# Kernel tuning notes

Hardware: AMD Instinct MI355X
Metric: run time of the kernel (lower is better)

The kernel has to match this reference:

```python
import jax, jax.numpy as jnp
import numpy as np

N = 100000
E = 1600000
F_IN = 128
HID = 64
N_CLS = 16


def gcn_conv(x, row, col, W, b, n_nodes):
    # x: [N, Fin]; row/col: [E+N] (self-loops already appended)
    h = x @ W  # [N, Fout]
    ones = jnp.ones(row.shape[0], dtype=x.dtype)
    deg = jax.ops.segment_sum(ones, col, num_segments=n_nodes)  # in-degree incl. self-loop
    dinv = jnp.where(deg > 0, jax.lax.rsqrt(deg), 0.0)
    norm = dinv[row] * dinv[col]  # [E+N]
    msg = h[row] * norm[:, None]  # gather + scale
    out = jax.ops.segment_sum(msg, col, num_segments=n_nodes)  # scatter-add
    return out + b


def setup_inputs() -> dict:
    key = jax.random.key(0)
    k1, k2, k3, k4, k5, k6 = jax.random.split(key, 6)
    x = jax.random.normal(k1, (N, F_IN), dtype=jnp.float32)
    edge_index = jax.random.randint(k2, (2, E), 0, N, dtype=jnp.int64)
    # Glorot-ish init for weights
    W1 = jax.random.normal(k3, (F_IN, HID), dtype=jnp.float32) / np.sqrt(F_IN)
    b1 = jnp.zeros((HID,), dtype=jnp.float32)
    W2 = jax.random.normal(k4, (HID, N_CLS), dtype=jnp.float32) / np.sqrt(HID)
    b2 = jnp.zeros((N_CLS,), dtype=jnp.float32)
    return {"x": x, "edge_index": edge_index, "W1": W1, "b1": b1, "W2": W2, "b2": b2}


def reference(x, edge_index, W1, b1, W2, b2):
    # Add self-loops (GCNConv default add_self_loops=True)
    loop = jnp.arange(N, dtype=edge_index.dtype)
    row = jnp.concatenate([edge_index[0], loop])
    col = jnp.concatenate([edge_index[1], loop])
    h = gcn_conv(x, row, col, W1, b1, N)
    h = jax.nn.relu(h)
    h = gcn_conv(h, row, col, W2, b2, N)
    return jax.nn.log_softmax(h, axis=1)
```

## Files before the change

kernel.cpp:

```cpp
#include <hip/hip_runtime.h>
#include <hip/hip_fp16.h>

#define F_IN 128
#define HID  64
#define NCLS 16
#define NPB  128
#define CHUNK 4096
#define BINTHREADS 1024
#define GPAD 136

typedef _Float16 half_t;
typedef __attribute__((ext_vector_type(4))) _Float16 half4;
typedef __attribute__((ext_vector_type(8))) _Float16 half8;
typedef __attribute__((ext_vector_type(4))) float float4v;


__global__ __launch_bounds__(BINTHREADS) void bucket_hist(const int* __restrict__ col,
                                                          int* __restrict__ tot, int E, int NB) {
    __shared__ int hist[1024];
    for (int i = threadIdx.x; i < NB; i += BINTHREADS) hist[i] = 0;
    __syncthreads();
    int e0 = blockIdx.x * CHUNK;
    #pragma unroll
    for (int j = 0; j < CHUNK / BINTHREADS; ++j) {
        int e = e0 + j * BINTHREADS + threadIdx.x;
        if (e < E) atomicAdd(&hist[col[e] >> 7], 1);
    }
    __syncthreads();
    for (int i = threadIdx.x; i < NB; i += BINTHREADS)
        if (hist[i]) atomicAdd(&tot[i], hist[i]);
}


__global__ __launch_bounds__(256) void bucket_scan(const int* __restrict__ tot,
                                                   int* __restrict__ base, int* __restrict__ cursor,
                                                   int* __restrict__ row_start, int NB, int N, int E) {
    __shared__ int s[256];
    int t = threadIdx.x, i0 = t * 4;
    int v0 = (i0 + 0 < NB) ? tot[i0 + 0] : 0;
    int v1 = (i0 + 1 < NB) ? tot[i0 + 1] : 0;
    int v2 = (i0 + 2 < NB) ? tot[i0 + 2] : 0;
    int v3 = (i0 + 3 < NB) ? tot[i0 + 3] : 0;
    int tsum = v0 + v1 + v2 + v3;
    s[t] = tsum;
    __syncthreads();
    for (int off = 1; off < 256; off <<= 1) {
        int x = (t >= off) ? s[t - off] : 0;
        __syncthreads();
        s[t] += x;
        __syncthreads();
    }
    int run = s[t] - tsum;
    if (i0 + 0 < NB) { base[i0 + 0] = run; cursor[i0 + 0] = run; } run += v0;
    if (i0 + 1 < NB) { base[i0 + 1] = run; cursor[i0 + 1] = run; } run += v1;
    if (i0 + 2 < NB) { base[i0 + 2] = run; cursor[i0 + 2] = run; } run += v2;
    if (i0 + 3 < NB) { base[i0 + 3] = run; cursor[i0 + 3] = run; }
    if (t == 0) { base[NB] = E; row_start[N] = E; }
}


__global__ __launch_bounds__(BINTHREADS) void phaseA(const int* __restrict__ row, const int* __restrict__ col,
                                                     int* __restrict__ cursor, int* __restrict__ ebuf,
                                                     int E, int NB) {
    __shared__ int hist[1024], base[1024], off[1024];
    for (int i = threadIdx.x; i < NB; i += BINTHREADS) hist[i] = 0;
    __syncthreads();
    int e0 = blockIdx.x * CHUNK;
    #pragma unroll
    for (int j = 0; j < CHUNK / BINTHREADS; ++j) {
        int e = e0 + j * BINTHREADS + threadIdx.x;
        if (e < E) atomicAdd(&hist[col[e] >> 7], 1);
    }
    __syncthreads();
    for (int i = threadIdx.x; i < NB; i += BINTHREADS) {
        int h = hist[i];
        base[i] = h ? atomicAdd(&cursor[i], h) : 0;
        off[i] = 0;
    }
    __syncthreads();
    #pragma unroll
    for (int j = 0; j < CHUNK / BINTHREADS; ++j) {
        int e = e0 + j * BINTHREADS + threadIdx.x;
        if (e < E) {
            int c = col[e], b = c >> 7;
            int p = base[b] + atomicAdd(&off[b], 1);
            ebuf[p] = (row[e] << 7) | (c & (NPB - 1));
        }
    }
}


__global__ __launch_bounds__(256) void phaseB(const int* __restrict__ ebuf, const int* __restrict__ bbase,
                                              int* __restrict__ row_start, int* __restrict__ csr_row,
                                              float* __restrict__ dinv, int N) {
    __shared__ int hist[NPB], sc[NPB], cur[NPB];
    int t = threadIdx.x;
    int node0 = blockIdx.x << 7;
    int e0 = bbase[blockIdx.x], e1 = bbase[blockIdx.x + 1];
    if (t < NPB) hist[t] = 0;
    __syncthreads();
    for (int e = e0 + t; e < e1; e += 256) atomicAdd(&hist[ebuf[e] & (NPB - 1)], 1);
    __syncthreads();
    if (t < NPB) sc[t] = hist[t];
    __syncthreads();
    for (int off = 1; off < NPB; off <<= 1) {
        int x = (t < NPB && t >= off) ? sc[t - off] : 0;
        __syncthreads();
        if (t < NPB) sc[t] += x;
        __syncthreads();
    }
    if (t < NPB) {
        int start = e0 + sc[t] - hist[t];
        cur[t] = start;
        int n = node0 + t;
        if (n < N) {
            row_start[n] = start;
            dinv[n] = rsqrtf((float)hist[t] + 1.0f);
        }
    }
    __syncthreads();
    for (int e = e0 + t; e < e1; e += 256) {
        int p = ebuf[e];
        int pos = atomicAdd(&cur[p & (NPB - 1)], 1);
        csr_row[pos] = p >> 7;
    }
}


__global__ void prep_w1(const float* __restrict__ W1, half_t* __restrict__ W1t) {
    int i = blockIdx.x * 256 + threadIdx.x;
    if (i < F_IN * HID) {
        int k = i >> 6, n = i & 63;
        W1t[n * F_IN + k] = (half_t)W1[i];
    }
}


__global__ __launch_bounds__(256) void gemm1(
    const float* __restrict__ x, const half_t* __restrict__ W1t,
    const float* __restrict__ dinv, __half* __restrict__ hs1, int N)
{
    __shared__ __align__(16) half_t As[16 * GPAD + 8];
    int node0 = blockIdx.x * 16;
    size_t total = (size_t)N * F_IN;
    for (int idx = threadIdx.x; idx < 16 * F_IN / 4; idx += 256) {
        int nl = idx >> 5;
        int k4 = idx & 31;
        size_t g = (size_t)(node0 + nl) * F_IN + k4 * 4;
        float4 v = make_float4(0.f, 0.f, 0.f, 0.f);
        if (g < total) v = *(const float4*)&x[g];
        half_t* dst = &As[nl * GPAD + k4 * 4];
        dst[0] = (half_t)v.x; dst[1] = (half_t)v.y;
        dst[2] = (half_t)v.z; dst[3] = (half_t)v.w;
    }
    __syncthreads();
    int wv = threadIdx.x >> 6, lane = threadIdx.x & 63;
    int l15 = lane & 15, quad = lane >> 4;
    int fcol = wv * 16 + l15;
    float4v acc = {0.f, 0.f, 0.f, 0.f};
    #pragma unroll
    for (int kb = 0; kb < 4; ++kb) {
        half8 a = *(const half8*)&As[l15 * GPAD + kb * 32 + quad * 8];
        half8 b = *(const half8*)&W1t[(size_t)fcol * F_IN + kb * 32 + quad * 8];
        acc = __builtin_amdgcn_mfma_f32_16x16x32_f16(a, b, acc, 0, 0, 0);
    }
    #pragma unroll
    for (int r = 0; r < 4; ++r) {
        int node = node0 + quad * 4 + r;
        if (node < N) hs1[(size_t)node * HID + fcol] = __float2half(acc[r] * dinv[node]);
    }
}


__global__ __launch_bounds__(256) void agg_l1(
    const __half* __restrict__ hs1, const int* __restrict__ rs,
    const int* __restrict__ csr, const float* __restrict__ dinv,
    const float* __restrict__ b1, const float* __restrict__ W2,
    __half* __restrict__ h2s, int N)
{
    __shared__ float W2l[HID * NCLS];
    __shared__ float o1[16][65];
    for (int i = threadIdx.x; i < HID * NCLS; i += 256) W2l[i] = W2[i];
    __syncthreads();
    int w = threadIdx.x >> 6, lane = threadIdx.x & 63;
    int g = lane >> 4, gl = lane & 15;
    int rowi = w * 4 + g;
    int c = blockIdx.x * 16 + rowi;
    bool active = (c < N);
    int cc = active ? c : 0;
    float dc = dinv[cc];
    int e0 = rs[cc], e1 = rs[cc + 1];
    int e1m1 = e1 - 1;
    const half4* H = (const half4*)hs1;
    half4 sv = H[(size_t)cc * 16 + gl];
    float4 sum = make_float4((float)sv[0], (float)sv[1], (float)sv[2], (float)sv[3]);
    for (int i = e0; i < e1; i += 8) {
        int id[8];
        #pragma unroll
        for (int s = 0; s < 8; ++s) id[s] = csr[min(i + s, e1m1)];
        half4 a[8];
        #pragma unroll
        for (int s = 0; s < 8; ++s) a[s] = H[(size_t)id[s] * 16 + gl];
        #pragma unroll
        for (int s = 0; s < 8; ++s) {
            float fm = (i + s < e1) ? 1.f : 0.f;
            sum.x = fmaf(fm, (float)a[s][0], sum.x);
            sum.y = fmaf(fm, (float)a[s][1], sum.y);
            sum.z = fmaf(fm, (float)a[s][2], sum.z);
            sum.w = fmaf(fm, (float)a[s][3], sum.w);
        }
    }
    float4 bb = *(const float4*)&b1[gl * 4];
    o1[rowi][gl * 4 + 0] = fmaxf(fmaf(dc, sum.x, bb.x), 0.f);
    o1[rowi][gl * 4 + 1] = fmaxf(fmaf(dc, sum.y, bb.y), 0.f);
    o1[rowi][gl * 4 + 2] = fmaxf(fmaf(dc, sum.z, bb.z), 0.f);
    o1[rowi][gl * 4 + 3] = fmaxf(fmaf(dc, sum.w, bb.w), 0.f);
    float s16 = 0.f;
    const float* orow = o1[rowi];
    #pragma unroll 8
    for (int k = 0; k < HID; ++k) s16 = fmaf(orow[k], W2l[k * NCLS + gl], s16);
    if (active) h2s[(size_t)c * NCLS + gl] = __float2half(dc * s16);
}


__global__ __launch_bounds__(256) void agg2_final(
    const __half* __restrict__ h2s, const int* __restrict__ rs,
    const int* __restrict__ csr, const float* __restrict__ dinv,
    const float* __restrict__ b2, float* __restrict__ out, int N)
{
    int lane = threadIdx.x & 63;
    int g = lane >> 3, gl = lane & 7;
    int c = blockIdx.x * 32 + (threadIdx.x >> 6) * 8 + g;
    bool active = (c < N);
    int cc = active ? c : 0;
    float dcv = dinv[cc];
    int e0 = rs[cc], e1 = rs[cc + 1];
    int e1m1 = e1 - 1;
    const __half2* H = (const __half2*)h2s;
    float2 sum = __half22float2(H[(size_t)cc * 8 + gl]);
    for (int i = e0; i < e1; i += 8) {
        int id[8];
        #pragma unroll
        for (int s = 0; s < 8; ++s) id[s] = csr[min(i + s, e1m1)];
        __half2 a[8];
        #pragma unroll
        for (int s = 0; s < 8; ++s) a[s] = H[(size_t)id[s] * 8 + gl];
        #pragma unroll
        for (int s = 0; s < 8; ++s) {
            float fm = (i + s < e1) ? 1.f : 0.f;
            float2 f2 = __half22float2(a[s]);
            sum.x = fmaf(fm, f2.x, sum.x);
            sum.y = fmaf(fm, f2.y, sum.y);
        }
    }
    float2 bb = ((const float2*)b2)[gl];
    float2 v;
    v.x = fmaf(dcv, sum.x, bb.x);
    v.y = fmaf(dcv, sum.y, bb.y);
    float mx = fmaxf(v.x, v.y);
    mx = fmaxf(mx, __shfl_xor(mx, 1, 64));
    mx = fmaxf(mx, __shfl_xor(mx, 2, 64));
    mx = fmaxf(mx, __shfl_xor(mx, 4, 64));
    float s = __expf(v.x - mx) + __expf(v.y - mx);
    s += __shfl_xor(s, 1, 64);
    s += __shfl_xor(s, 2, 64);
    s += __shfl_xor(s, 4, 64);
    float lse = mx + __logf(s);
    if (active) ((float2*)out)[(size_t)c * 8 + gl] = make_float2(v.x - lse, v.y - lse);
}


extern "C" void kernel_launch(void* const* d_in, const int* in_sizes, int n_in,
                              void* d_out, int out_size, void* d_ws, size_t ws_size,
                              hipStream_t stream) {
    const float* x  = (const float*)d_in[0];
    const int*   ei = (const int*)d_in[1];
    const float* W1 = (const float*)d_in[2];
    const float* b1 = (const float*)d_in[3];
    const float* W2 = (const float*)d_in[4];
    const float* b2 = (const float*)d_in[5];
    float* out = (float*)d_out;

    const int N = in_sizes[0] / F_IN;
    const int E = in_sizes[1] / 2;
    const int* row = ei;
    const int* col = ei + E;

    const int NB = (N + NPB - 1) / NPB;
    size_t Np  = ((size_t)N + 15) & ~(size_t)15;
    size_t Ep  = ((size_t)E + 15) & ~(size_t)15;
    size_t NBp = ((size_t)NB + 15) & ~(size_t)15;

    char* p = (char*)d_ws;
    float*  dinv      = (float*)p;   p += Np * 4;
    __half* hs1       = (__half*)p;  p += Np * HID * 2;
    __half* h2s       = (__half*)p;  p += Np * NCLS * 2;
    half_t* W1t       = (half_t*)p;  p += (size_t)F_IN * HID * 2;
    int*    row_start = (int*)p;     p += (Np + 16) * 4;
    int*    csr_row   = (int*)p;     p += Ep * 4;
    int*    ebuf      = (int*)p;     p += Ep * 4;
    int*    btot      = (int*)p;     p += NBp * 4;
    int*    bbase     = (int*)p;     p += (NBp + 16) * 4;
    int*    bcur      = (int*)p;     p += NBp * 4;

    int nblkE = (E + CHUNK - 1) / CHUNK;

    hipMemsetAsync(btot, 0, NBp * sizeof(int), stream);
    bucket_hist<<<nblkE, BINTHREADS, 0, stream>>>(col, btot, E, NB);
    bucket_scan<<<1, 256, 0, stream>>>(btot, bbase, bcur, row_start, NB, N, E);
    phaseA<<<nblkE, BINTHREADS, 0, stream>>>(row, col, bcur, ebuf, E, NB);
    phaseB<<<NB, 256, 0, stream>>>(ebuf, bbase, row_start, csr_row, dinv, N);
    prep_w1<<<(F_IN * HID + 255) / 256, 256, 0, stream>>>(W1, W1t);
    gemm1<<<(N + 15) / 16, 256, 0, stream>>>(x, W1t, dinv, hs1, N);
    agg_l1<<<(N + 15) / 16, 256, 0, stream>>>(hs1, row_start, csr_row, dinv, b1, W2, h2s, N);
    agg2_final<<<(N + 31) / 32, 256, 0, stream>>>(h2s, row_start, csr_row, dinv, b2, out, N);
}
```

Measured before the change: 210.5 us.

## Fold W1 prep into histogram, shuffle scan, wider gemm1 and agg_l1 tiles

```diff
diff --git a/kernel.cpp b/kernel.cpp
--- a/kernel.cpp
+++ b/kernel.cpp
@@ -10,13 +10,21 @@
 #define GPAD 136
 
 typedef _Float16 half_t;
-typedef __attribute__((ext_vector_type(4))) _Float16 half4;
 typedef __attribute__((ext_vector_type(8))) _Float16 half8;
 typedef __attribute__((ext_vector_type(4))) float float4v;
 
 
-__global__ __launch_bounds__(BINTHREADS) void bucket_hist(const int* __restrict__ col,
-                                                          int* __restrict__ tot, int E, int NB) {
+__global__ __launch_bounds__(BINTHREADS) void bucket_hist(
+    const int* __restrict__ col, int* __restrict__ tot, int E, int NB,
+    const float* __restrict__ W1, half_t* __restrict__ W1t, int nblkE)
+{
+    if ((int)blockIdx.x >= nblkE) {
+        for (int i = threadIdx.x; i < F_IN * HID; i += BINTHREADS) {
+            int k = i >> 6, n = i & 63;
+            W1t[n * F_IN + k] = (half_t)W1[i];
+        }
+        return;
+    }
     __shared__ int hist[1024];
     for (int i = threadIdx.x; i < NB; i += BINTHREADS) hist[i] = 0;
     __syncthreads();
@@ -93,7 +101,8 @@
 __global__ __launch_bounds__(256) void phaseB(const int* __restrict__ ebuf, const int* __restrict__ bbase,
                                               int* __restrict__ row_start, int* __restrict__ csr_row,
                                               float* __restrict__ dinv, int N) {
-    __shared__ int hist[NPB], sc[NPB], cur[NPB];
+    __shared__ int hist[NPB], cur[NPB];
+    __shared__ int wtot;
     int t = threadIdx.x;
     int node0 = blockIdx.x << 7;
     int e0 = bbase[blockIdx.x], e1 = bbase[blockIdx.x + 1];
@@ -101,21 +110,26 @@
     __syncthreads();
     for (int e = e0 + t; e < e1; e += 256) atomicAdd(&hist[ebuf[e] & (NPB - 1)], 1);
     __syncthreads();
-    if (t < NPB) sc[t] = hist[t];
-    __syncthreads();
-    for (int off = 1; off < NPB; off <<= 1) {
-        int x = (t < NPB && t >= off) ? sc[t - off] : 0;
-        __syncthreads();
-        if (t < NPB) sc[t] += x;
-        __syncthreads();
-    }
+    int h = 0, incl = 0;
     if (t < NPB) {
-        int start = e0 + sc[t] - hist[t];
+        h = hist[t];
+        incl = h;
+        #pragma unroll
+        for (int off = 1; off < 64; off <<= 1) {
+            int u = __shfl_up(incl, off, 64);
+            if ((t & 63) >= off) incl += u;
+        }
+        if (t == 63) wtot = incl;
+    }
+    __syncthreads();
+    if (t < NPB) {
+        if (t >= 64) incl += wtot;
+        int start = e0 + incl - h;
         cur[t] = start;
         int n = node0 + t;
         if (n < N) {
             row_start[n] = start;
-            dinv[n] = rsqrtf((float)hist[t] + 1.0f);
+            dinv[n] = rsqrtf((float)h + 1.0f);
         }
     }
     __syncthreads();
@@ -127,23 +141,14 @@
 }
 
 
-__global__ void prep_w1(const float* __restrict__ W1, half_t* __restrict__ W1t) {
-    int i = blockIdx.x * 256 + threadIdx.x;
-    if (i < F_IN * HID) {
-        int k = i >> 6, n = i & 63;
-        W1t[n * F_IN + k] = (half_t)W1[i];
-    }
-}
-
-
 __global__ __launch_bounds__(256) void gemm1(
     const float* __restrict__ x, const half_t* __restrict__ W1t,
     const float* __restrict__ dinv, __half* __restrict__ hs1, int N)
 {
-    __shared__ __align__(16) half_t As[16 * GPAD + 8];
-    int node0 = blockIdx.x * 16;
+    __shared__ __align__(16) half_t As[32 * GPAD + 8];
+    int node0 = blockIdx.x * 32;
     size_t total = (size_t)N * F_IN;
-    for (int idx = threadIdx.x; idx < 16 * F_IN / 4; idx += 256) {
+    for (int idx = threadIdx.x; idx < 32 * F_IN / 4; idx += 256) {
         int nl = idx >> 5;
         int k4 = idx & 31;
         size_t g = (size_t)(node0 + nl) * F_IN + k4 * 4;
@@ -157,17 +162,22 @@
     int wv = threadIdx.x >> 6, lane = threadIdx.x & 63;
     int l15 = lane & 15, quad = lane >> 4;
     int fcol = wv * 16 + l15;
-    float4v acc = {0.f, 0.f, 0.f, 0.f};
+    float4v acc0 = {0.f, 0.f, 0.f, 0.f};
+    float4v acc1 = {0.f, 0.f, 0.f, 0.f};
     #pragma unroll
     for (int kb = 0; kb < 4; ++kb) {
-        half8 a = *(const half8*)&As[l15 * GPAD + kb * 32 + quad * 8];
-        half8 b = *(const half8*)&W1t[(size_t)fcol * F_IN + kb * 32 + quad * 8];
-        acc = __builtin_amdgcn_mfma_f32_16x16x32_f16(a, b, acc, 0, 0, 0);
+        half8 b  = *(const half8*)&W1t[(size_t)fcol * F_IN + kb * 32 + quad * 8];
+        half8 a0 = *(const half8*)&As[l15 * GPAD + kb * 32 + quad * 8];
+        half8 a1 = *(const half8*)&As[(16 + l15) * GPAD + kb * 32 + quad * 8];
+        acc0 = __builtin_amdgcn_mfma_f32_16x16x32_f16(a0, b, acc0, 0, 0, 0);
+        acc1 = __builtin_amdgcn_mfma_f32_16x16x32_f16(a1, b, acc1, 0, 0, 0);
     }
     #pragma unroll
     for (int r = 0; r < 4; ++r) {
-        int node = node0 + quad * 4 + r;
-        if (node < N) hs1[(size_t)node * HID + fcol] = __float2half(acc[r] * dinv[node]);
+        int n0 = node0 + quad * 4 + r;
+        int n1 = n0 + 16;
+        if (n0 < N) hs1[(size_t)n0 * HID + fcol] = __float2half(acc0[r] * dinv[n0]);
+        if (n1 < N) hs1[(size_t)n1 * HID + fcol] = __float2half(acc1[r] * dinv[n1]);
     }
 }
 
@@ -179,47 +189,62 @@
     __half* __restrict__ h2s, int N)
 {
     __shared__ float W2l[HID * NCLS];
-    __shared__ float o1[16][65];
+    __shared__ float o1[32][65];
     for (int i = threadIdx.x; i < HID * NCLS; i += 256) W2l[i] = W2[i];
     __syncthreads();
     int w = threadIdx.x >> 6, lane = threadIdx.x & 63;
-    int g = lane >> 4, gl = lane & 15;
-    int rowi = w * 4 + g;
-    int c = blockIdx.x * 16 + rowi;
+    int g = lane >> 3, gl = lane & 7;
+    int rowi = w * 8 + g;
+    int c = blockIdx.x * 32 + rowi;
     bool active = (c < N);
     int cc = active ? c : 0;
     float dc = dinv[cc];
     int e0 = rs[cc], e1 = rs[cc + 1];
     int e1m1 = e1 - 1;
-    const half4* H = (const half4*)hs1;
-    half4 sv = H[(size_t)cc * 16 + gl];
-    float4 sum = make_float4((float)sv[0], (float)sv[1], (float)sv[2], (float)sv[3]);
+    const half8* H = (const half8*)hs1;
+    half8 sv = H[(size_t)cc * 8 + gl];
+    float sum[8];
+    #pragma unroll
+    for (int k = 0; k < 8; ++k) sum[k] = (float)sv[k];
     for (int i = e0; i < e1; i += 8) {
         int id[8];
         #pragma unroll
         for (int s = 0; s < 8; ++s) id[s] = csr[min(i + s, e1m1)];
-        half4 a[8];
-        #pragma unroll
-        for (int s = 0; s < 8; ++s) a[s] = H[(size_t)id[s] * 16 + gl];
+        half8 a[8];
+        #pragma unroll
+        for (int s = 0; s < 8; ++s) a[s] = H[(size_t)id[s] * 8 + gl];
         #pragma unroll
         for (int s = 0; s < 8; ++s) {
             float fm = (i + s < e1) ? 1.f : 0.f;
-            sum.x = fmaf(fm, (float)a[s][0], sum.x);
-            sum.y = fmaf(fm, (float)a[s][1], sum.y);
-            sum.z = fmaf(fm, (float)a[s][2], sum.z);
-            sum.w = fmaf(fm, (float)a[s][3], sum.w);
-        }
-    }
-    float4 bb = *(const float4*)&b1[gl * 4];
-    o1[rowi][gl * 4 + 0] = fmaxf(fmaf(dc, sum.x, bb.x), 0.f);
-    o1[rowi][gl * 4 + 1] = fmaxf(fmaf(dc, sum.y, bb.y), 0.f);
-    o1[rowi][gl * 4 + 2] = fmaxf(fmaf(dc, sum.z, bb.z), 0.f);
-    o1[rowi][gl * 4 + 3] = fmaxf(fmaf(dc, sum.w, bb.w), 0.f);
-    float s16 = 0.f;
+            #pragma unroll
+            for (int k = 0; k < 8; ++k) sum[k] = fmaf(fm, (float)a[s][k], sum[k]);
+        }
+    }
+    float4 bb0 = *(const float4*)&b1[gl * 8];
+    float4 bb1 = *(const float4*)&b1[gl * 8 + 4];
+    o1[rowi][gl * 8 + 0] = fmaxf(fmaf(dc, sum[0], bb0.x), 0.f);
+    o1[rowi][gl * 8 + 1] = fmaxf(fmaf(dc, sum[1], bb0.y), 0.f);
+    o1[rowi][gl * 8 + 2] = fmaxf(fmaf(dc, sum[2], bb0.z), 0.f);
+    o1[rowi][gl * 8 + 3] = fmaxf(fmaf(dc, sum[3], bb0.w), 0.f);
+    o1[rowi][gl * 8 + 4] = fmaxf(fmaf(dc, sum[4], bb1.x), 0.f);
+    o1[rowi][gl * 8 + 5] = fmaxf(fmaf(dc, sum[5], bb1.y), 0.f);
+    o1[rowi][gl * 8 + 6] = fmaxf(fmaf(dc, sum[6], bb1.z), 0.f);
+    o1[rowi][gl * 8 + 7] = fmaxf(fmaf(dc, sum[7], bb1.w), 0.f);
+    int j0 = gl * 2, j1 = gl * 2 + 1;
+    float s0 = 0.f, s1 = 0.f;
     const float* orow = o1[rowi];
     #pragma unroll 8
-    for (int k = 0; k < HID; ++k) s16 = fmaf(orow[k], W2l[k * NCLS + gl], s16);
-    if (active) h2s[(size_t)c * NCLS + gl] = __float2half(dc * s16);
+    for (int k = 0; k < HID; ++k) {
+        float ov = orow[k];
+        s0 = fmaf(ov, W2l[k * NCLS + j0], s0);
+        s1 = fmaf(ov, W2l[k * NCLS + j1], s1);
+    }
+    if (active) {
+        __half2 hv;
+        hv.x = __float2half(dc * s0);
+        hv.y = __float2half(dc * s1);
+        ((__half2*)h2s)[(size_t)c * 8 + gl] = hv;
+    }
 }
 
 
@@ -306,12 +331,11 @@
     int nblkE = (E + CHUNK - 1) / CHUNK;
 
     hipMemsetAsync(btot, 0, NBp * sizeof(int), stream);
-    bucket_hist<<<nblkE, BINTHREADS, 0, stream>>>(col, btot, E, NB);
+    bucket_hist<<<nblkE + 1, BINTHREADS, 0, stream>>>(col, btot, E, NB, W1, W1t, nblkE);
     bucket_scan<<<1, 256, 0, stream>>>(btot, bbase, bcur, row_start, NB, N, E);
     phaseA<<<nblkE, BINTHREADS, 0, stream>>>(row, col, bcur, ebuf, E, NB);
     phaseB<<<NB, 256, 0, stream>>>(ebuf, bbase, row_start, csr_row, dinv, N);
-    prep_w1<<<(F_IN * HID + 255) / 256, 256, 0, stream>>>(W1, W1t);
-    gemm1<<<(N + 15) / 16, 256, 0, stream>>>(x, W1t, dinv, hs1, N);
-    agg_l1<<<(N + 15) / 16, 256, 0, stream>>>(hs1, row_start, csr_row, dinv, b1, W2, h2s, N);
+    gemm1<<<(N + 31) / 32, 256, 0, stream>>>(x, W1t, dinv, hs1, N);
+    agg_l1<<<(N + 31) / 32, 256, 0, stream>>>(hs1, row_start, csr_row, dinv, b1, W2, h2s, N);
     agg2_final<<<(N + 31) / 32, 256, 0, stream>>>(h2s, row_start, csr_row, dinv, b2, out, N);
 }
```

New measurement: 207.2 us. No clear change (-1.5%).
